# Performance work log

Measured on AMD Instinct MI355X. Metric: run time of the kernel, lower is better.

The kernel has to match this reference:

```python
import jax, jax.numpy as jnp
import numpy as np

N = 50000
E = 800000
NUM_GRAPHS = 64
D_IN = 261
D_SAGE = 64
D_LIN = 32
N_SAGE_REST = 6
N_LIN_REST = 3
EPS = 1e-5


def _layernorm(x, g, b):
    mu = jnp.mean(x, axis=-1, keepdims=True)
    var = jnp.mean((x - mu) ** 2, axis=-1, keepdims=True)
    return (x - mu) * jax.lax.rsqrt(var + EPS) * g + b


def _sage_block(x, Wl, bl, Wr, g, b, src, dst, inv_deg, residual):
    # mean aggregation of neighbor (source) features onto targets
    msum = jax.ops.segment_sum(x[src], dst, num_segments=N)  # [N, d]
    mean = msum * inv_deg  # [N, d]
    f = mean @ Wl + bl + x @ Wr  # lin_l(aggr) + lin_r(x); lin_r has no bias
    f = jax.nn.gelu(f, approximate=False)
    f = _layernorm(f, g, b)
    if residual:
        f = f + x
    return f


def _lin_block(x, W, b, g, beta, residual):
    f = jax.nn.gelu(x @ W + b, approximate=False)
    f = _layernorm(f, g, beta)
    if residual:
        f = f + x
    return f


def setup_inputs() -> dict:
    key = jax.random.key(0)
    ks = jax.random.split(key, 24)
    x = jax.random.normal(ks[0], (N, D_IN), dtype=jnp.float32)
    edge_index = jax.random.randint(ks[1], (2, E), 0, N, dtype=jnp.int64)
    batch = jnp.sort(jax.random.randint(ks[2], (N,), 0, NUM_GRAPHS, dtype=jnp.int64))

    def glorot(k, shape):
        fan_in = shape[0]
        return jax.random.normal(k, shape, dtype=jnp.float32) / np.sqrt(fan_in)

    inp = {
        "x": x, "edge_index": edge_index, "batch": batch,
        # first SAGE block (261 -> 64, no residual)
        "Wl0": glorot(ks[3], (D_IN, D_SAGE)), "bl0": jnp.zeros((D_SAGE,), jnp.float32),
        "Wr0": glorot(ks[4], (D_IN, D_SAGE)),
        "g0": jnp.ones((D_SAGE,), jnp.float32), "beta0": jnp.zeros((D_SAGE,), jnp.float32),
        # 6 residual SAGE blocks (64 -> 64), stacked
        "Wl": glorot(ks[5], (N_SAGE_REST, D_SAGE, D_SAGE)),
        "bl": jnp.zeros((N_SAGE_REST, D_SAGE), jnp.float32),
        "Wr": glorot(ks[6], (N_SAGE_REST, D_SAGE, D_SAGE)),
        "g": jnp.ones((N_SAGE_REST, D_SAGE), jnp.float32),
        "beta": jnp.zeros((N_SAGE_REST, D_SAGE), jnp.float32),
        # MLP: first LinearBlock 64 -> 32 (no residual)
        "M0": glorot(ks[7], (D_SAGE, D_LIN)), "mb0": jnp.zeros((D_LIN,), jnp.float32),
        "mg0": jnp.ones((D_LIN,), jnp.float32), "mbeta0": jnp.zeros((D_LIN,), jnp.float32),
        # 3 residual LinearBlocks 32 -> 32, stacked
        "M": glorot(ks[8], (N_LIN_REST, D_LIN, D_LIN)),
        "mb": jnp.zeros((N_LIN_REST, D_LIN), jnp.float32),
        "mg": jnp.ones((N_LIN_REST, D_LIN), jnp.float32),
        "mbeta": jnp.zeros((N_LIN_REST, D_LIN), jnp.float32),
        # final Linear 32 -> 1
        "Wf": glorot(ks[9], (D_LIN, 1)), "bf": jnp.zeros((1,), jnp.float32),
    }
    return inp


def reference(x, edge_index, batch, Wl0, bl0, Wr0, g0, beta0, Wl, bl, Wr, g, beta,
              M0, mb0, mg0, mbeta0, M, mb, mg, mbeta, Wf, bf):
    src, dst = edge_index[0], edge_index[1]
    deg = jax.ops.segment_sum(jnp.ones((E,), x.dtype), dst, num_segments=N)
    inv_deg = (1.0 / jnp.maximum(deg, 1.0))[:, None]  # [N,1]

    h = _sage_block(x, Wl0, bl0, Wr0, g0, beta0, src, dst, inv_deg, residual=False)
    for i in range(N_SAGE_REST):
        h = _sage_block(h, Wl[i], bl[i], Wr[i], g[i], beta[i], src, dst, inv_deg, residual=True)

    pooled = jax.ops.segment_sum(h, batch, num_segments=NUM_GRAPHS)  # [G, 64]

    m = _lin_block(pooled, M0, mb0, mg0, mbeta0, residual=False)
    for i in range(N_LIN_REST):
        m = _lin_block(m, M[i], mb[i], mg[i], mbeta[i], residual=True)
    return m @ Wf + bf  # [G, 1]
```

## Files before the change

### kernel.cpp

```cpp
#include <hip/hip_runtime.h>
#include <hip/hip_bf16.h>
#include <math.h>

#define N_NODES 50000
#define N_EDGES 800000
#define NUM_GRAPHS 64
#define NPAD 50048
#define KPAD0 288
#define PSPLIT 16
#define MAXDEG 64

#define G0_GRID    (NPAD / 32)
#define LAYER_GRID (NPAD / 32)
#define PREPW_TOT  (128 * KPAD0 + 6 * 128 * 64)
#define PREPW_GRID ((PREPW_TOT + 255) / 256)
#define CONV_GRID  (NPAD * (KPAD0 / 8) / 256)
#define PREP2_GRID (CONV_GRID + PREPW_GRID)

#define SLICES 8
#define NPS 6250
#define SCHUNK 2048
#define SCHUNKS ((N_EDGES + SCHUNK - 1) / SCHUNK)
#define SCAT_SPLIT 196

typedef __attribute__((ext_vector_type(8))) short short8;
typedef __attribute__((ext_vector_type(4))) float f32x4;

__device__ __forceinline__ float gelu_f(float v) {
    return 0.5f * v * (1.0f + erff(v * 0.70710678118654752440f));
}

__device__ __forceinline__ float half_sum32(float v) {
    v += __shfl_xor(v, 1); v += __shfl_xor(v, 2); v += __shfl_xor(v, 4);
    v += __shfl_xor(v, 8); v += __shfl_xor(v, 16);
    return v;
}

__device__ __forceinline__ float group_sum8(float v) {
    v += __shfl_xor(v, 1); v += __shfl_xor(v, 2); v += __shfl_xor(v, 4);
    return v;
}

__device__ __forceinline__ unsigned short f2bf(float f) {
    unsigned int u = __float_as_uint(f);
    unsigned int r = (u + 0x7fffu + ((u >> 16) & 1u)) >> 16;
    return (unsigned short)r;
}

__device__ __forceinline__ float bf_lo(unsigned int u) {
    return __uint_as_float(u << 16);
}
__device__ __forceinline__ float bf_hi(unsigned int u) {
    return __uint_as_float(u & 0xffff0000u);
}


__global__ __launch_bounds__(256) void k_prep2(
        const float* __restrict__ X, unsigned short* __restrict__ Xbf,
        const float* __restrict__ Wl0, const float* __restrict__ Wr0,
        const float* __restrict__ Wl, const float* __restrict__ Wr,
        unsigned short* __restrict__ Bt0, unsigned short* __restrict__ BtR) {
    const int blk = blockIdx.x;
    const int tid = threadIdx.x;
    if (blk < CONV_GRID) {
        int t = blk * 256 + tid;
        int node = t / (KPAD0 / 8);
        int k8 = (t - node * (KPAD0 / 8)) * 8;
        short8 v8;
        if (node < N_NODES) {
            #pragma unroll
            for (int j = 0; j < 8; ++j) {
                int k = k8 + j;
                float val = (k < 261) ? __builtin_nontemporal_load(&X[(size_t)node * 261 + k]) : 0.0f;
                v8[j] = (short)f2bf(val);
            }
        } else {
            #pragma unroll
            for (int j = 0; j < 8; ++j) v8[j] = 0;
        }
        *(short8*)&Xbf[(size_t)node * KPAD0 + k8] = v8;
        return;
    }
    int idx = (blk - CONV_GRID) * 256 + tid;
    const int n0 = 128 * KPAD0;
    if (idx < n0) {
        int j = idx / KPAD0, k = idx - j * KPAD0;
        float v = 0.0f;
        if (k < 261) v = (j < 64) ? Wl0[k * 64 + j] : Wr0[k * 64 + (j - 64)];
        Bt0[idx] = f2bf(v);
    } else if (idx < PREPW_TOT) {
        int r = idx - n0;
        int l = r >> 13;
        int rr = r & 8191;
        int j = rr >> 6, k = rr & 63;
        float v = (j < 64) ? Wl[l * 4096 + k * 64 + j] : Wr[l * 4096 + k * 64 + (j - 64)];
        BtR[r] = f2bf(v);
    }
}


__global__ __launch_bounds__(256) void k_scat(
        int cbase,
        const int* __restrict__ src, const int* __restrict__ dst,
        int* __restrict__ deg, unsigned short* __restrict__ col64) {
    const int sid = cbase * 8 + blockIdx.x;
    const int s = sid & (SLICES - 1);
    const int c = sid >> 3;
    const int base = c * SCHUNK;
    const int lim = min(base + SCHUNK, N_EDGES);
    for (int i = base + (int)threadIdx.x; i < lim; i += 256) {
        int d = __builtin_nontemporal_load(&dst[i]);
        if (d / NPS == s) {
            int sv = __builtin_nontemporal_load(&src[i]);
            int pos = atomicAdd(&deg[d], 1);
            if (pos < MAXDEG) col64[(d << 6) + pos] = (unsigned short)sv;
        }
    }
}


__global__ __launch_bounds__(256) void k_gemm0(
        const unsigned short* __restrict__ Xbf, const unsigned short* __restrict__ Bt0,
        unsigned short* __restrict__ U, float* __restrict__ V) {
    __shared__ __align__(16) unsigned short sB[64 * 296];
    const int tid = threadIdx.x;
    const int lane = tid & 63, wid = tid >> 6;
    const int l16 = lane & 15, quad = lane >> 4;
    const int ch = blockIdx.x & 1;
    const int m0 = (blockIdx.x >> 1) * 64;
    #pragma unroll
    for (int k = 0; k < 9; ++k) {
        int g = k * 256 + tid;
        int row = g / 36;
        int part = (g - row * 36) * 8;
        *(short8*)&sB[row * 296 + part] =
            *(const short8*)&Bt0[(size_t)(ch * 64 + row) * KPAD0 + part];
    }
    f32x4 acc[4];
    #pragma unroll
    for (int j = 0; j < 4; ++j) { acc[j][0] = 0.f; acc[j][1] = 0.f; acc[j][2] = 0.f; acc[j][3] = 0.f; }
    const unsigned short* xr = Xbf + (size_t)(m0 + wid * 16 + l16) * KPAD0 + quad * 8;
    __syncthreads();
    for (int kc = 0; kc < KPAD0; kc += 32) {
        short8 af = *(const short8*)(xr + kc);
        #pragma unroll
        for (int j = 0; j < 4; ++j) {
            short8 bfv = *(const short8*)&sB[(j * 16 + l16) * 296 + kc + quad * 8];
            acc[j] = __builtin_amdgcn_mfma_f32_16x16x32_bf16(af, bfv, acc[j], 0, 0, 0);
        }
    }
    const int rbase = m0 + wid * 16 + quad * 4;
    if (ch == 0) {
        #pragma unroll
        for (int j = 0; j < 4; ++j)
            #pragma unroll
            for (int r = 0; r < 4; ++r)
                U[(size_t)(rbase + r) * 64 + j * 16 + l16] = f2bf(acc[j][r]);
    } else {
        #pragma unroll
        for (int j = 0; j < 4; ++j)
            #pragma unroll
            for (int r = 0; r < 4; ++r)
                V[(size_t)(rbase + r) * 64 + j * 16 + l16] = acc[j][r];
    }
}


__global__ __launch_bounds__(256) void k_layer(
        const unsigned short* __restrict__ U_in, const float* __restrict__ V_in,
        unsigned short* __restrict__ h,
        const int* __restrict__ deg, const unsigned short* __restrict__ col64,
        const float* __restrict__ bias, const float* __restrict__ gam,
        const float* __restrict__ bet,
        const unsigned short* __restrict__ Bt_next,
        unsigned short* __restrict__ U_out, float* __restrict__ V_out,
        const int* __restrict__ batch, float* __restrict__ pool_part,
        int residual, int have_gemm) {
    __shared__ __align__(16) unsigned short sA[2 * 32 * 32];
    __shared__ __align__(16) unsigned short sB[128 * 72];
    const int tid = threadIdx.x;
    const int lane = tid & 63, wid = tid >> 6;
    const int sub = lane >> 3, hl = lane & 7;
    const int base = lane & 56;
    const int m0 = blockIdx.x * 32;
    const uint4* __restrict__ Up = (const uint4*)U_in;

    if (have_gemm) {
        #pragma unroll
        for (int k = 0; k < 4; ++k) {
            int g = k * 256 + tid;
            int row = g >> 3, part = (g & 7) * 8;
            *(short8*)&sB[row * 72 + part] = *(const short8*)&Bt_next[(size_t)row * 64 + part];
        }
    }

    const int nl = wid * 8 + sub;
    const int node = m0 + nl;
    const bool valid = (node < N_NODES);
    const int nd = valid ? node : 0;
    const int dg = valid ? deg[nd] : 0;
    const int cnt = min(dg, MAXDEG);
    uint4 cv = make_uint4(0u, 0u, 0u, 0u);
    if (valid) cv = *(const uint4*)&col64[((size_t)nd << 6) + hl * 8];

    float4 v0 = make_float4(0.f, 0.f, 0.f, 0.f), v1 = v0;
    if (valid) {
        v0 = *(const float4*)&V_in[(size_t)nd * 64 + 8 * hl];
        v1 = *(const float4*)&V_in[(size_t)nd * 64 + 8 * hl + 4];
    }
    uint4 hu = make_uint4(0u, 0u, 0u, 0u);
    if (residual && valid) hu = ((const uint4*)h)[(size_t)nd * 8 + hl];

    float s0 = 0.f, s1 = 0.f, s2 = 0.f, s3 = 0.f, s4 = 0.f, s5 = 0.f, s6 = 0.f, s7 = 0.f;
    for (int b = 0; b * 8 < cnt; b += 2) {
        #pragma unroll
        for (int hh = 0; hh < 2; ++hh) {
            const int sl = base + b + hh;
            unsigned int p0 = (unsigned int)__shfl((int)cv.x, sl);
            unsigned int p1 = (unsigned int)__shfl((int)cv.y, sl);
            unsigned int p2 = (unsigned int)__shfl((int)cv.z, sl);
            unsigned int p3 = (unsigned int)__shfl((int)cv.w, sl);
            const int eb = (b + hh) * 8;
            int c[8];
            c[0] = (int)(p0 & 0xffffu); c[1] = (int)(p0 >> 16);
            c[2] = (int)(p1 & 0xffffu); c[3] = (int)(p1 >> 16);
            c[4] = (int)(p2 & 0xffffu); c[5] = (int)(p2 >> 16);
            c[6] = (int)(p3 & 0xffffu); c[7] = (int)(p3 >> 16);
            #pragma unroll
            for (int i = 0; i < 8; ++i) {
                uint4 u = (eb + i < cnt) ? Up[(size_t)c[i] * 8 + hl] : make_uint4(0u, 0u, 0u, 0u);
                s0 += bf_lo(u.x); s1 += bf_hi(u.x);
                s2 += bf_lo(u.y); s3 += bf_hi(u.y);
                s4 += bf_lo(u.z); s5 += bf_hi(u.z);
                s6 += bf_lo(u.w); s7 += bf_hi(u.w);
            }
        }
    }
    const float id = 1.0f / fmaxf((float)dg, 1.0f);
    const float4 b0 = *(const float4*)&bias[8 * hl];
    const float4 b1 = *(const float4*)&bias[8 * hl + 4];
    float f0 = gelu_f(s0 * id + b0.x + v0.x);
    float f1 = gelu_f(s1 * id + b0.y + v0.y);
    float f2 = gelu_f(s2 * id + b0.z + v0.z);
    float f3 = gelu_f(s3 * id + b0.w + v0.w);
    float f4 = gelu_f(s4 * id + b1.x + v1.x);
    float f5 = gelu_f(s5 * id + b1.y + v1.y);
    float f6 = gelu_f(s6 * id + b1.z + v1.z);
    float f7 = gelu_f(s7 * id + b1.w + v1.w);
    float mu = group_sum8(((f0 + f1) + (f2 + f3)) + ((f4 + f5) + (f6 + f7))) * 0.015625f;
    float d0 = f0 - mu, d1 = f1 - mu, d2 = f2 - mu, d3 = f3 - mu;
    float d4 = f4 - mu, d5 = f5 - mu, d6 = f6 - mu, d7 = f7 - mu;
    float var = group_sum8(((d0 * d0 + d1 * d1) + (d2 * d2 + d3 * d3)) +
                           ((d4 * d4 + d5 * d5) + (d6 * d6 + d7 * d7))) * 0.015625f;
    float rs = rsqrtf(var + 1e-5f);
    const float4 g0v = *(const float4*)&gam[8 * hl];
    const float4 g1v = *(const float4*)&gam[8 * hl + 4];
    const float4 e0v = *(const float4*)&bet[8 * hl];
    const float4 e1v = *(const float4*)&bet[8 * hl + 4];
    f0 = d0 * rs * g0v.x + e0v.x;
    f1 = d1 * rs * g0v.y + e0v.y;
    f2 = d2 * rs * g0v.z + e0v.z;
    f3 = d3 * rs * g0v.w + e0v.w;
    f4 = d4 * rs * g1v.x + e1v.x;
    f5 = d5 * rs * g1v.y + e1v.y;
    f6 = d6 * rs * g1v.z + e1v.z;
    f7 = d7 * rs * g1v.w + e1v.w;
    if (residual && valid) {
        f0 += bf_lo(hu.x); f1 += bf_hi(hu.x);
        f2 += bf_lo(hu.y); f3 += bf_hi(hu.y);
        f4 += bf_lo(hu.z); f5 += bf_hi(hu.z);
        f6 += bf_lo(hu.w); f7 += bf_hi(hu.w);
    }

    if (pool_part) {
        const int myg = valid ? batch[nd] : -1;
        const int i_lo = (m0 < N_NODES) ? m0 : (N_NODES - 1);
        const int i_hi = (m0 + 31 < N_NODES) ? (m0 + 31) : (N_NODES - 1);
        const int g_lo = batch[i_lo];
        const int g_hi = batch[i_hi];
        const int split = blockIdx.x & (PSPLIT - 1);
        for (int g = g_lo; g <= g_hi; ++g) {
            const bool mine = (myg == g);
            float p0 = mine ? f0 : 0.f, p1 = mine ? f1 : 0.f;
            float p2 = mine ? f2 : 0.f, p3 = mine ? f3 : 0.f;
            float p4 = mine ? f4 : 0.f, p5 = mine ? f5 : 0.f;
            float p6 = mine ? f6 : 0.f, p7 = mine ? f7 : 0.f;
            p0 += __shfl_xor(p0, 8);  p1 += __shfl_xor(p1, 8);
            p2 += __shfl_xor(p2, 8);  p3 += __shfl_xor(p3, 8);
            p4 += __shfl_xor(p4, 8);  p5 += __shfl_xor(p5, 8);
            p6 += __shfl_xor(p6, 8);  p7 += __shfl_xor(p7, 8);
            p0 += __shfl_xor(p0, 16); p1 += __shfl_xor(p1, 16);
            p2 += __shfl_xor(p2, 16); p3 += __shfl_xor(p3, 16);
            p4 += __shfl_xor(p4, 16); p5 += __shfl_xor(p5, 16);
            p6 += __shfl_xor(p6, 16); p7 += __shfl_xor(p7, 16);
            p0 += __shfl_xor(p0, 32); p1 += __shfl_xor(p1, 32);
            p2 += __shfl_xor(p2, 32); p3 += __shfl_xor(p3, 32);
            p4 += __shfl_xor(p4, 32); p5 += __shfl_xor(p5, 32);
            p6 += __shfl_xor(p6, 32); p7 += __shfl_xor(p7, 32);
            if (sub == 0) {
                float* dp = &pool_part[((size_t)g * PSPLIT + split) * 64 + 8 * hl];
                atomicAdd(dp + 0, p0); atomicAdd(dp + 1, p1);
                atomicAdd(dp + 2, p2); atomicAdd(dp + 3, p3);
                atomicAdd(dp + 4, p4); atomicAdd(dp + 5, p5);
                atomicAdd(dp + 6, p6); atomicAdd(dp + 7, p7);
            }
        }
        return;
    }

    uint4 outw;
    outw.x = (unsigned int)f2bf(f0) | ((unsigned int)f2bf(f1) << 16);
    outw.y = (unsigned int)f2bf(f2) | ((unsigned int)f2bf(f3) << 16);
    outw.z = (unsigned int)f2bf(f4) | ((unsigned int)f2bf(f5) << 16);
    outw.w = (unsigned int)f2bf(f6) | ((unsigned int)f2bf(f7) << 16);
    if (valid) ((uint4*)h)[(size_t)nd * 8 + hl] = outw;
    *(uint4*)&sA[(((hl >> 2) * 32 + nl) << 5) + (hl & 3) * 8] = outw;

    if (!have_gemm) return;
    __syncthreads();

    const int l16 = lane & 15, quad = lane >> 4;
    const int wrow = wid & 1, colh = wid >> 1;
    f32x4 acc[4];
    #pragma unroll
    for (int j = 0; j < 4; ++j) { acc[j][0] = 0.f; acc[j][1] = 0.f; acc[j][2] = 0.f; acc[j][3] = 0.f; }
    #pragma unroll
    for (int kc = 0; kc < 64; kc += 32) {
        short8 af = *(const short8*)&sA[(((kc >> 5) * 32 + wrow * 16 + l16) << 5) + quad * 8];
        #pragma unroll
        for (int j = 0; j < 4; ++j) {
            short8 bfv = *(const short8*)&sB[(colh * 64 + j * 16 + l16) * 72 + kc + quad * 8];
            acc[j] = __builtin_amdgcn_mfma_f32_16x16x32_bf16(af, bfv, acc[j], 0, 0, 0);
        }
    }
    const int rbase = m0 + wrow * 16 + quad * 4;
    if (colh == 0) {
        #pragma unroll
        for (int j = 0; j < 4; ++j)
            #pragma unroll
            for (int r = 0; r < 4; ++r)
                U_out[(size_t)(rbase + r) * 64 + j * 16 + l16] = f2bf(acc[j][r]);
    } else {
        #pragma unroll
        for (int j = 0; j < 4; ++j)
            #pragma unroll
            for (int r = 0; r < 4; ++r)
                V_out[(size_t)(rbase + r) * 64 + j * 16 + l16] = acc[j][r];
    }
}


__global__ __launch_bounds__(1024) void k_head(const float* __restrict__ partial,
                                               const float* __restrict__ M0, const float* __restrict__ mb0,
                                               const float* __restrict__ mg0, const float* __restrict__ mbeta0,
                                               const float* __restrict__ M, const float* __restrict__ mb,
                                               const float* __restrict__ mg, const float* __restrict__ mbeta,
                                               const float* __restrict__ Wf, const float* __restrict__ bf,
                                               float* __restrict__ out) {
    __shared__ float sP[64 * 64];
    __shared__ float sA[64 * 33];
    __shared__ float sB[64 * 33];
    const int tx = threadIdx.x, ty = threadIdx.y;
    const int tid = ty * 32 + tx;
    for (int i = tid; i < 64 * 64; i += 1024) {
        int g = i >> 6, f = i & 63;
        float s = 0.0f;
        #pragma unroll
        for (int s2 = 0; s2 < PSPLIT; ++s2) s += partial[(size_t)(g * PSPLIT + s2) * 64 + f];
        sP[i] = s;
    }
    __syncthreads();
    #pragma unroll
    for (int rr = 0; rr < 2; ++rr) {
        int r = ty + rr * 32;
        float a = mb0[tx];
        for (int k = 0; k < 64; ++k) a += sP[r * 64 + k] * M0[k * 32 + tx];
        a = gelu_f(a);
        float mu = half_sum32(a) * (1.0f / 32.0f);
        float d = a - mu;
        float var = half_sum32(d * d) * (1.0f / 32.0f);
        a = d * rsqrtf(var + 1e-5f) * mg0[tx] + mbeta0[tx];
        sA[r * 33 + tx] = a;
    }
    __syncthreads();
    float* cur = sA;
    float* nxt = sB;
    for (int L = 0; L < 3; ++L) {
        const float* Mi = M + L * 32 * 32;
        const float* mbi = mb + L * 32;
        const float* mgi = mg + L * 32;
        const float* mbetai = mbeta + L * 32;
        #pragma unroll
        for (int rr = 0; rr < 2; ++rr) {
            int r = ty + rr * 32;
            float a = mbi[tx];
            for (int k = 0; k < 32; ++k) a += cur[r * 33 + k] * Mi[k * 32 + tx];
            a = gelu_f(a);
            float mu = half_sum32(a) * (1.0f / 32.0f);
            float d = a - mu;
            float var = half_sum32(d * d) * (1.0f / 32.0f);
            a = d * rsqrtf(var + 1e-5f) * mgi[tx] + mbetai[tx] + cur[r * 33 + tx];
            nxt[r * 33 + tx] = a;
        }
        __syncthreads();
        float* t = cur; cur = nxt; nxt = t;
    }
    #pragma unroll
    for (int rr = 0; rr < 2; ++rr) {
        int r = ty + rr * 32;
        float p = cur[r * 33 + tx] * Wf[tx];
        p = half_sum32(p);
        if (tx == 0) out[r] = p + bf[0];
    }
}


extern "C" void kernel_launch(void* const* d_in, const int* in_sizes, int n_in,
                              void* d_out, int out_size, void* d_ws, size_t ws_size,
                              hipStream_t stream) {
    const int N = N_NODES;
    const int E = N_EDGES;

    const float* x    = (const float*)d_in[0];
    const int* eidx   = (const int*)d_in[1];
    const int* batch  = (const int*)d_in[2];
    const float* Wl0  = (const float*)d_in[3];
    const float* bl0  = (const float*)d_in[4];
    const float* Wr0  = (const float*)d_in[5];
    const float* g0   = (const float*)d_in[6];
    const float* bet0 = (const float*)d_in[7];
    const float* Wl   = (const float*)d_in[8];
    const float* bl   = (const float*)d_in[9];
    const float* Wr   = (const float*)d_in[10];
    const float* gR   = (const float*)d_in[11];
    const float* betR = (const float*)d_in[12];
    const float* M0   = (const float*)d_in[13];
    const float* mb0  = (const float*)d_in[14];
    const float* mg0  = (const float*)d_in[15];
    const float* mbe0 = (const float*)d_in[16];
    const float* M    = (const float*)d_in[17];
    const float* mb   = (const float*)d_in[18];
    const float* mg   = (const float*)d_in[19];
    const float* mbe  = (const float*)d_in[20];
    const float* Wf   = (const float*)d_in[21];
    const float* bf   = (const float*)d_in[22];

    const int* src = eidx;
    const int* dst = eidx + E;

    char* p = (char*)d_ws;
    auto alloc = [&](size_t bytes) -> void* {
        void* q = (void*)p;
        p += (bytes + 255) & ~(size_t)255;
        return q;
    };
    int*   deg     = (int*)alloc((size_t)N * 4);
    float* partial = (float*)alloc((size_t)NUM_GRAPHS * PSPLIT * 64 * 4);
    unsigned short* col64 = (unsigned short*)alloc((size_t)N * MAXDEG * 2);
    unsigned short* Bt0 = (unsigned short*)alloc((size_t)128 * KPAD0 * 2);
    unsigned short* BtR = (unsigned short*)alloc((size_t)6 * 128 * 64 * 2);
    unsigned short* Xbf = (unsigned short*)alloc((size_t)NPAD * KPAD0 * 2);
    unsigned short* Ua  = (unsigned short*)alloc((size_t)NPAD * 64 * 2);
    unsigned short* Ub  = (unsigned short*)alloc((size_t)NPAD * 64 * 2);
    float* Va   = (float*)alloc((size_t)NPAD * 64 * 4);
    float* Vb   = (float*)alloc((size_t)NPAD * 64 * 4);
    unsigned short* hbuf = (unsigned short*)alloc((size_t)NPAD * 64 * 2);

    size_t zspan = (size_t)((char*)col64 - (char*)deg);
    hipMemsetAsync(deg, 0, zspan, stream);

    k_prep2<<<PREP2_GRID, 256, 0, stream>>>(x, Xbf, Wl0, Wr0, Wl, Wr, Bt0, BtR);

    k_scat<<<SCAT_SPLIT * 8, 256, 0, stream>>>(0, src, dst, deg, col64);
    k_scat<<<(SCHUNKS - SCAT_SPLIT) * 8, 256, 0, stream>>>(SCAT_SPLIT, src, dst, deg, col64);

    k_gemm0<<<G0_GRID, 256, 0, stream>>>(Xbf, Bt0, Ua, Va);

    unsigned short* Uin = Ua;  float* Vin = Va;
    unsigned short* Uout = Ub; float* Vout = Vb;
    for (int i = 0; i < 7; ++i) {
        const float* bias = (i == 0) ? bl0  : bl  + (size_t)(i - 1) * 64;
        const float* gam  = (i == 0) ? g0   : gR  + (size_t)(i - 1) * 64;
        const float* bet  = (i == 0) ? bet0 : betR + (size_t)(i - 1) * 64;
        const int have_gemm = (i < 6);
        float* pool_part = (i == 6) ? partial : nullptr;
        k_layer<<<LAYER_GRID, 256, 0, stream>>>(
            Uin, Vin, hbuf, deg, col64, bias, gam, bet,
            have_gemm ? (BtR + (size_t)i * 128 * 64) : BtR,
            Uout, Vout, batch, pool_part, (i > 0) ? 1 : 0, have_gemm);
        unsigned short* tu = Uin; Uin = Uout; Uout = tu;
        float* tv = Vin; Vin = Vout; Vout = tv;
    }

    k_head<<<1, dim3(32, 32), 0, stream>>>(partial, M0, mb0, mg0, mbe0, M, mb, mg, mbe, Wf, bf, (float*)d_out);
}
```

Measured before the change: 415.7 us.

## Fuse seven per-layer SAGE kernels into one persistent cooperative kernel with grid sync

Replaces the seven separate layer launches with one cooperative persistent kernel that loops over layers, processes node tiles in a grid-stride loop, and uses grid.sync between layers. It also merges the two scatter launches into one. The aim is to remove per-launch overhead and tail effects between layers. In exchange, the grid is capped by occupancy, tiles are processed serially per block, and a grid-wide barrier is added per layer.

```diff
diff --git a/kernel.cpp b/kernel.cpp
--- a/kernel.cpp
+++ b/kernel.cpp
@@ -1,4 +1,5 @@
 #include <hip/hip_runtime.h>
+#include <hip/hip_cooperative_groups.h>
 #include <hip/hip_bf16.h>
 #include <math.h>
 
@@ -11,7 +12,7 @@
 #define MAXDEG 64
 
 #define G0_GRID    (NPAD / 32)
-#define LAYER_GRID (NPAD / 32)
+#define LAYER_TILES (NPAD / 32)
 #define PREPW_TOT  (128 * KPAD0 + 6 * 128 * 64)
 #define PREPW_GRID ((PREPW_TOT + 255) / 256)
 #define CONV_GRID  (NPAD * (KPAD0 / 8) / 256)
@@ -21,7 +22,9 @@
 #define NPS 6250
 #define SCHUNK 2048
 #define SCHUNKS ((N_EDGES + SCHUNK - 1) / SCHUNK)
-#define SCAT_SPLIT 196
+#define SCAT_GRID (SCHUNKS * SLICES)
+
+namespace cg = cooperative_groups;
 
 typedef __attribute__((ext_vector_type(8))) short short8;
 typedef __attribute__((ext_vector_type(4))) float f32x4;
@@ -100,12 +103,10 @@
 
 
 __global__ __launch_bounds__(256) void k_scat(
-        int cbase,
         const int* __restrict__ src, const int* __restrict__ dst,
         int* __restrict__ deg, unsigned short* __restrict__ col64) {
-    const int sid = cbase * 8 + blockIdx.x;
-    const int s = sid & (SLICES - 1);
-    const int c = sid >> 3;
+    const int s = blockIdx.x & (SLICES - 1);
+    const int c = blockIdx.x >> 3;
     const int base = c * SCHUNK;
     const int lim = min(base + SCHUNK, N_EDGES);
     for (int i = base + (int)threadIdx.x; i < lim; i += 256) {
@@ -166,186 +167,202 @@
 }
 
 
-__global__ __launch_bounds__(256) void k_layer(
-        const unsigned short* __restrict__ U_in, const float* __restrict__ V_in,
+__global__ __launch_bounds__(256) void k_net(
+        unsigned short* __restrict__ Ua, float* __restrict__ Va,
+        unsigned short* __restrict__ Ub, float* __restrict__ Vb,
         unsigned short* __restrict__ h,
         const int* __restrict__ deg, const unsigned short* __restrict__ col64,
-        const float* __restrict__ bias, const float* __restrict__ gam,
-        const float* __restrict__ bet,
-        const unsigned short* __restrict__ Bt_next,
-        unsigned short* __restrict__ U_out, float* __restrict__ V_out,
-        const int* __restrict__ batch, float* __restrict__ pool_part,
-        int residual, int have_gemm) {
+        const float* __restrict__ bl0, const float* __restrict__ g0,
+        const float* __restrict__ bet0,
+        const float* __restrict__ blR, const float* __restrict__ gR,
+        const float* __restrict__ betR,
+        const unsigned short* __restrict__ BtR,
+        const int* __restrict__ batch, float* __restrict__ partial) {
     __shared__ __align__(16) unsigned short sA[2 * 32 * 32];
     __shared__ __align__(16) unsigned short sB[128 * 72];
+    cg::grid_group grid = cg::this_grid();
     const int tid = threadIdx.x;
     const int lane = tid & 63, wid = tid >> 6;
     const int sub = lane >> 3, hl = lane & 7;
     const int base = lane & 56;
-    const int m0 = blockIdx.x * 32;
-    const uint4* __restrict__ Up = (const uint4*)U_in;
-
-    if (have_gemm) {
-        #pragma unroll
-        for (int k = 0; k < 4; ++k) {
-            int g = k * 256 + tid;
-            int row = g >> 3, part = (g & 7) * 8;
-            *(short8*)&sB[row * 72 + part] = *(const short8*)&Bt_next[(size_t)row * 64 + part];
-        }
-    }
-
-    const int nl = wid * 8 + sub;
-    const int node = m0 + nl;
-    const bool valid = (node < N_NODES);
-    const int nd = valid ? node : 0;
-    const int dg = valid ? deg[nd] : 0;
-    const int cnt = min(dg, MAXDEG);
-    uint4 cv = make_uint4(0u, 0u, 0u, 0u);
-    if (valid) cv = *(const uint4*)&col64[((size_t)nd << 6) + hl * 8];
-
-    float4 v0 = make_float4(0.f, 0.f, 0.f, 0.f), v1 = v0;
-    if (valid) {
-        v0 = *(const float4*)&V_in[(size_t)nd * 64 + 8 * hl];
-        v1 = *(const float4*)&V_in[(size_t)nd * 64 + 8 * hl + 4];
-    }
-    uint4 hu = make_uint4(0u, 0u, 0u, 0u);
-    if (residual && valid) hu = ((const uint4*)h)[(size_t)nd * 8 + hl];
-
-    float s0 = 0.f, s1 = 0.f, s2 = 0.f, s3 = 0.f, s4 = 0.f, s5 = 0.f, s6 = 0.f, s7 = 0.f;
-    for (int b = 0; b * 8 < cnt; b += 2) {
-        #pragma unroll
-        for (int hh = 0; hh < 2; ++hh) {
-            const int sl = base + b + hh;
-            unsigned int p0 = (unsigned int)__shfl((int)cv.x, sl);
-            unsigned int p1 = (unsigned int)__shfl((int)cv.y, sl);
-            unsigned int p2 = (unsigned int)__shfl((int)cv.z, sl);
-            unsigned int p3 = (unsigned int)__shfl((int)cv.w, sl);
-            const int eb = (b + hh) * 8;
-            int c[8];
-            c[0] = (int)(p0 & 0xffffu); c[1] = (int)(p0 >> 16);
-            c[2] = (int)(p1 & 0xffffu); c[3] = (int)(p1 >> 16);
-            c[4] = (int)(p2 & 0xffffu); c[5] = (int)(p2 >> 16);
-            c[6] = (int)(p3 & 0xffffu); c[7] = (int)(p3 >> 16);
+
+    for (int L = 0; L < 7; ++L) {
+        const int have_gemm = (L < 6);
+        const int residual = (L > 0);
+        const unsigned short* U_in = (L & 1) ? Ub : Ua;
+        const float* V_in = (L & 1) ? Vb : Va;
+        unsigned short* U_out = (L & 1) ? Ua : Ub;
+        float* V_out = (L & 1) ? Va : Vb;
+        const float* bias = L ? (blR + (size_t)(L - 1) * 64) : bl0;
+        const float* gam  = L ? (gR  + (size_t)(L - 1) * 64) : g0;
+        const float* bet  = L ? (betR + (size_t)(L - 1) * 64) : bet0;
+        const uint4* __restrict__ Up = (const uint4*)U_in;
+
+        if (have_gemm) {
+            const unsigned short* Bt = BtR + (size_t)L * 128 * 64;
             #pragma unroll
-            for (int i = 0; i < 8; ++i) {
-                uint4 u = (eb + i < cnt) ? Up[(size_t)c[i] * 8 + hl] : make_uint4(0u, 0u, 0u, 0u);
-                s0 += bf_lo(u.x); s1 += bf_hi(u.x);
-                s2 += bf_lo(u.y); s3 += bf_hi(u.y);
-                s4 += bf_lo(u.z); s5 += bf_hi(u.z);
-                s6 += bf_lo(u.w); s7 += bf_hi(u.w);
+            for (int k = 0; k < 4; ++k) {
+                int g = k * 256 + tid;
+                int row = g >> 3, part = (g & 7) * 8;
+                *(short8*)&sB[row * 72 + part] = *(const short8*)&Bt[(size_t)row * 64 + part];
             }
         }
-    }
-    const float id = 1.0f / fmaxf((float)dg, 1.0f);
-    const float4 b0 = *(const float4*)&bias[8 * hl];
-    const float4 b1 = *(const float4*)&bias[8 * hl + 4];
-    float f0 = gelu_f(s0 * id + b0.x + v0.x);
-    float f1 = gelu_f(s1 * id + b0.y + v0.y);
-    float f2 = gelu_f(s2 * id + b0.z + v0.z);
-    float f3 = gelu_f(s3 * id + b0.w + v0.w);
-    float f4 = gelu_f(s4 * id + b1.x + v1.x);
-    float f5 = gelu_f(s5 * id + b1.y + v1.y);
-    float f6 = gelu_f(s6 * id + b1.z + v1.z);
-    float f7 = gelu_f(s7 * id + b1.w + v1.w);
-    float mu = group_sum8(((f0 + f1) + (f2 + f3)) + ((f4 + f5) + (f6 + f7))) * 0.015625f;
-    float d0 = f0 - mu, d1 = f1 - mu, d2 = f2 - mu, d3 = f3 - mu;
-    float d4 = f4 - mu, d5 = f5 - mu, d6 = f6 - mu, d7 = f7 - mu;
-    float var = group_sum8(((d0 * d0 + d1 * d1) + (d2 * d2 + d3 * d3)) +
-                           ((d4 * d4 + d5 * d5) + (d6 * d6 + d7 * d7))) * 0.015625f;
-    float rs = rsqrtf(var + 1e-5f);
-    const float4 g0v = *(const float4*)&gam[8 * hl];
-    const float4 g1v = *(const float4*)&gam[8 * hl + 4];
-    const float4 e0v = *(const float4*)&bet[8 * hl];
-    const float4 e1v = *(const float4*)&bet[8 * hl + 4];
-    f0 = d0 * rs * g0v.x + e0v.x;
-    f1 = d1 * rs * g0v.y + e0v.y;
-    f2 = d2 * rs * g0v.z + e0v.z;
-    f3 = d3 * rs * g0v.w + e0v.w;
-    f4 = d4 * rs * g1v.x + e1v.x;
-    f5 = d5 * rs * g1v.y + e1v.y;
-    f6 = d6 * rs * g1v.z + e1v.z;
-    f7 = d7 * rs * g1v.w + e1v.w;
-    if (residual && valid) {
-        f0 += bf_lo(hu.x); f1 += bf_hi(hu.x);
-        f2 += bf_lo(hu.y); f3 += bf_hi(hu.y);
-        f4 += bf_lo(hu.z); f5 += bf_hi(hu.z);
-        f6 += bf_lo(hu.w); f7 += bf_hi(hu.w);
-    }
-
-    if (pool_part) {
-        const int myg = valid ? batch[nd] : -1;
-        const int i_lo = (m0 < N_NODES) ? m0 : (N_NODES - 1);
-        const int i_hi = (m0 + 31 < N_NODES) ? (m0 + 31) : (N_NODES - 1);
-        const int g_lo = batch[i_lo];
-        const int g_hi = batch[i_hi];
-        const int split = blockIdx.x & (PSPLIT - 1);
-        for (int g = g_lo; g <= g_hi; ++g) {
-            const bool mine = (myg == g);
-            float p0 = mine ? f0 : 0.f, p1 = mine ? f1 : 0.f;
-            float p2 = mine ? f2 : 0.f, p3 = mine ? f3 : 0.f;
-            float p4 = mine ? f4 : 0.f, p5 = mine ? f5 : 0.f;
-            float p6 = mine ? f6 : 0.f, p7 = mine ? f7 : 0.f;
-            p0 += __shfl_xor(p0, 8);  p1 += __shfl_xor(p1, 8);
-            p2 += __shfl_xor(p2, 8);  p3 += __shfl_xor(p3, 8);
-            p4 += __shfl_xor(p4, 8);  p5 += __shfl_xor(p5, 8);
-            p6 += __shfl_xor(p6, 8);  p7 += __shfl_xor(p7, 8);
-            p0 += __shfl_xor(p0, 16); p1 += __shfl_xor(p1, 16);
-            p2 += __shfl_xor(p2, 16); p3 += __shfl_xor(p3, 16);
-            p4 += __shfl_xor(p4, 16); p5 += __shfl_xor(p5, 16);
-            p6 += __shfl_xor(p6, 16); p7 += __shfl_xor(p7, 16);
-            p0 += __shfl_xor(p0, 32); p1 += __shfl_xor(p1, 32);
-            p2 += __shfl_xor(p2, 32); p3 += __shfl_xor(p3, 32);
-            p4 += __shfl_xor(p4, 32); p5 += __shfl_xor(p5, 32);
-            p6 += __shfl_xor(p6, 32); p7 += __shfl_xor(p7, 32);
-            if (sub == 0) {
-                float* dp = &pool_part[((size_t)g * PSPLIT + split) * 64 + 8 * hl];
-                atomicAdd(dp + 0, p0); atomicAdd(dp + 1, p1);
-                atomicAdd(dp + 2, p2); atomicAdd(dp + 3, p3);
-                atomicAdd(dp + 4, p4); atomicAdd(dp + 5, p5);
-                atomicAdd(dp + 6, p6); atomicAdd(dp + 7, p7);
+
+        for (int tile = blockIdx.x; tile < LAYER_TILES; tile += gridDim.x) {
+            const int m0 = tile * 32;
+            const int nl = wid * 8 + sub;
+            const int node = m0 + nl;
+            const bool valid = (node < N_NODES);
+            const int nd = valid ? node : 0;
+            const int dg = valid ? deg[nd] : 0;
+            const int cnt = min(dg, MAXDEG);
+            uint4 cv = make_uint4(0u, 0u, 0u, 0u);
+            if (valid) cv = *(const uint4*)&col64[((size_t)nd << 6) + hl * 8];
+
+            float4 v0 = make_float4(0.f, 0.f, 0.f, 0.f), v1 = v0;
+            if (valid) {
+                v0 = *(const float4*)&V_in[(size_t)nd * 64 + 8 * hl];
+                v1 = *(const float4*)&V_in[(size_t)nd * 64 + 8 * hl + 4];
+            }
+            uint4 hu = make_uint4(0u, 0u, 0u, 0u);
+            if (residual && valid) hu = ((const uint4*)h)[(size_t)nd * 8 + hl];
+
+            float s0 = 0.f, s1 = 0.f, s2 = 0.f, s3 = 0.f, s4 = 0.f, s5 = 0.f, s6 = 0.f, s7 = 0.f;
+            for (int b = 0; b * 8 < cnt; b += 2) {
+                #pragma unroll
+                for (int hh = 0; hh < 2; ++hh) {
+                    const int sl = base + b + hh;
+                    unsigned int p0 = (unsigned int)__shfl((int)cv.x, sl);
+                    unsigned int p1 = (unsigned int)__shfl((int)cv.y, sl);
+                    unsigned int p2 = (unsigned int)__shfl((int)cv.z, sl);
+                    unsigned int p3 = (unsigned int)__shfl((int)cv.w, sl);
+                    const int eb = (b + hh) * 8;
+                    int c[8];
+                    c[0] = (int)(p0 & 0xffffu); c[1] = (int)(p0 >> 16);
+                    c[2] = (int)(p1 & 0xffffu); c[3] = (int)(p1 >> 16);
+                    c[4] = (int)(p2 & 0xffffu); c[5] = (int)(p2 >> 16);
+                    c[6] = (int)(p3 & 0xffffu); c[7] = (int)(p3 >> 16);
+                    #pragma unroll
+                    for (int i = 0; i < 8; ++i) {
+                        uint4 u = (eb + i < cnt) ? Up[(size_t)c[i] * 8 + hl] : make_uint4(0u, 0u, 0u, 0u);
+                        s0 += bf_lo(u.x); s1 += bf_hi(u.x);
+                        s2 += bf_lo(u.y); s3 += bf_hi(u.y);
+                        s4 += bf_lo(u.z); s5 += bf_hi(u.z);
+                        s6 += bf_lo(u.w); s7 += bf_hi(u.w);
+                    }
+                }
+            }
+            const float id = 1.0f / fmaxf((float)dg, 1.0f);
+            const float4 b0 = *(const float4*)&bias[8 * hl];
+            const float4 b1 = *(const float4*)&bias[8 * hl + 4];
+            float f0 = gelu_f(s0 * id + b0.x + v0.x);
+            float f1 = gelu_f(s1 * id + b0.y + v0.y);
+            float f2 = gelu_f(s2 * id + b0.z + v0.z);
+            float f3 = gelu_f(s3 * id + b0.w + v0.w);
+            float f4 = gelu_f(s4 * id + b1.x + v1.x);
+            float f5 = gelu_f(s5 * id + b1.y + v1.y);
+            float f6 = gelu_f(s6 * id + b1.z + v1.z);
+            float f7 = gelu_f(s7 * id + b1.w + v1.w);
+            float mu = group_sum8(((f0 + f1) + (f2 + f3)) + ((f4 + f5) + (f6 + f7))) * 0.015625f;
+            float d0 = f0 - mu, d1 = f1 - mu, d2 = f2 - mu, d3 = f3 - mu;
+            float d4 = f4 - mu, d5 = f5 - mu, d6 = f6 - mu, d7 = f7 - mu;
+            float var = group_sum8(((d0 * d0 + d1 * d1) + (d2 * d2 + d3 * d3)) +
+                                   ((d4 * d4 + d5 * d5) + (d6 * d6 + d7 * d7))) * 0.015625f;
+            float rs = rsqrtf(var + 1e-5f);
+            const float4 g0v = *(const float4*)&gam[8 * hl];
+            const float4 g1v = *(const float4*)&gam[8 * hl + 4];
+            const float4 e0v = *(const float4*)&bet[8 * hl];
+            const float4 e1v = *(const float4*)&bet[8 * hl + 4];
+            f0 = d0 * rs * g0v.x + e0v.x;
+            f1 = d1 * rs * g0v.y + e0v.y;
+            f2 = d2 * rs * g0v.z + e0v.z;
+            f3 = d3 * rs * g0v.w + e0v.w;
+            f4 = d4 * rs * g1v.x + e1v.x;
+            f5 = d5 * rs * g1v.y + e1v.y;
+            f6 = d6 * rs * g1v.z + e1v.z;
+            f7 = d7 * rs * g1v.w + e1v.w;
+            if (residual && valid) {
+                f0 += bf_lo(hu.x); f1 += bf_hi(hu.x);
+                f2 += bf_lo(hu.y); f3 += bf_hi(hu.y);
+                f4 += bf_lo(hu.z); f5 += bf_hi(hu.z);
+                f6 += bf_lo(hu.w); f7 += bf_hi(hu.w);
+            }
+
+            if (L == 6) {
+                const int myg = valid ? batch[nd] : -1;
+                const int i_lo = (m0 < N_NODES) ? m0 : (N_NODES - 1);
+                const int i_hi = (m0 + 31 < N_NODES) ? (m0 + 31) : (N_NODES - 1);
+                const int g_lo = batch[i_lo];
+                const int g_hi = batch[i_hi];
+                const int split = tile & (PSPLIT - 1);
+                for (int g = g_lo; g <= g_hi; ++g) {
+                    const bool mine = (myg == g);
+                    float p0 = mine ? f0 : 0.f, p1 = mine ? f1 : 0.f;
+                    float p2 = mine ? f2 : 0.f, p3 = mine ? f3 : 0.f;
+                    float p4 = mine ? f4 : 0.f, p5 = mine ? f5 : 0.f;
+                    float p6 = mine ? f6 : 0.f, p7 = mine ? f7 : 0.f;
+                    p0 += __shfl_xor(p0, 8);  p1 += __shfl_xor(p1, 8);
+                    p2 += __shfl_xor(p2, 8);  p3 += __shfl_xor(p3, 8);
+                    p4 += __shfl_xor(p4, 8);  p5 += __shfl_xor(p5, 8);
+                    p6 += __shfl_xor(p6, 8);  p7 += __shfl_xor(p7, 8);
+                    p0 += __shfl_xor(p0, 16); p1 += __shfl_xor(p1, 16);
+                    p2 += __shfl_xor(p2, 16); p3 += __shfl_xor(p3, 16);
+                    p4 += __shfl_xor(p4, 16); p5 += __shfl_xor(p5, 16);
+                    p6 += __shfl_xor(p6, 16); p7 += __shfl_xor(p7, 16);
+                    p0 += __shfl_xor(p0, 32); p1 += __shfl_xor(p1, 32);
+                    p2 += __shfl_xor(p2, 32); p3 += __shfl_xor(p3, 32);
+                    p4 += __shfl_xor(p4, 32); p5 += __shfl_xor(p5, 32);
+                    p6 += __shfl_xor(p6, 32); p7 += __shfl_xor(p7, 32);
+                    if (sub == 0) {
+                        float* dp = &partial[((size_t)g * PSPLIT + split) * 64 + 8 * hl];
+                        atomicAdd(dp + 0, p0); atomicAdd(dp + 1, p1);
+                        atomicAdd(dp + 2, p2); atomicAdd(dp + 3, p3);
+                        atomicAdd(dp + 4, p4); atomicAdd(dp + 5, p5);
+                        atomicAdd(dp + 6, p6); atomicAdd(dp + 7, p7);
+                    }
+                }
+            } else {
+                uint4 outw;
+                outw.x = (unsigned int)f2bf(f0) | ((unsigned int)f2bf(f1) << 16);
+                outw.y = (unsigned int)f2bf(f2) | ((unsigned int)f2bf(f3) << 16);
+                outw.z = (unsigned int)f2bf(f4) | ((unsigned int)f2bf(f5) << 16);
+                outw.w = (unsigned int)f2bf(f6) | ((unsigned int)f2bf(f7) << 16);
+                if (valid) ((uint4*)h)[(size_t)nd * 8 + hl] = outw;
+                *(uint4*)&sA[(((hl >> 2) * 32 + nl) << 5) + (hl & 3) * 8] = outw;
+                __syncthreads();
+
+                const int l16 = lane & 15, quad = lane >> 4;
+                const int wrow = wid & 1, colh = wid >> 1;
+                f32x4 acc[4];
+                #pragma unroll
+                for (int j = 0; j < 4; ++j) { acc[j][0] = 0.f; acc[j][1] = 0.f; acc[j][2] = 0.f; acc[j][3] = 0.f; }
+                #pragma unroll
+                for (int kc = 0; kc < 64; kc += 32) {
+                    short8 af = *(const short8*)&sA[(((kc >> 5) * 32 + wrow * 16 + l16) << 5) + quad * 8];
+                    #pragma unroll
+                    for (int j = 0; j < 4; ++j) {
+                        short8 bfv = *(const short8*)&sB[(colh * 64 + j * 16 + l16) * 72 + kc + quad * 8];
+                        acc[j] = __builtin_amdgcn_mfma_f32_16x16x32_bf16(af, bfv, acc[j], 0, 0, 0);
+                    }
+                }
+                const int rbase = m0 + wrow * 16 + quad * 4;
+                if (colh == 0) {
+                    #pragma unroll
+                    for (int j = 0; j < 4; ++j)
+                        #pragma unroll
+                        for (int r = 0; r < 4; ++r)
+                            U_out[(size_t)(rbase + r) * 64 + j * 16 + l16] = f2bf(acc[j][r]);
+                } else {
+                    #pragma unroll
+                    for (int j = 0; j < 4; ++j)
+                        #pragma unroll
+                        for (int r = 0; r < 4; ++r)
+                            V_out[(size_t)(rbase + r) * 64 + j * 16 + l16] = acc[j][r];
+                }
+                __syncthreads();
             }
         }
-        return;
-    }
-
-    uint4 outw;
-    outw.x = (unsigned int)f2bf(f0) | ((unsigned int)f2bf(f1) << 16);
-    outw.y = (unsigned int)f2bf(f2) | ((unsigned int)f2bf(f3) << 16);
-    outw.z = (unsigned int)f2bf(f4) | ((unsigned int)f2bf(f5) << 16);
-    outw.w = (unsigned int)f2bf(f6) | ((unsigned int)f2bf(f7) << 16);
-    if (valid) ((uint4*)h)[(size_t)nd * 8 + hl] = outw;
-    *(uint4*)&sA[(((hl >> 2) * 32 + nl) << 5) + (hl & 3) * 8] = outw;
-
-    if (!have_gemm) return;
-    __syncthreads();
-
-    const int l16 = lane & 15, quad = lane >> 4;
-    const int wrow = wid & 1, colh = wid >> 1;
-    f32x4 acc[4];
-    #pragma unroll
-    for (int j = 0; j < 4; ++j) { acc[j][0] = 0.f; acc[j][1] = 0.f; acc[j][2] = 0.f; acc[j][3] = 0.f; }
-    #pragma unroll
-    for (int kc = 0; kc < 64; kc += 32) {
-        short8 af = *(const short8*)&sA[(((kc >> 5) * 32 + wrow * 16 + l16) << 5) + quad * 8];
-        #pragma unroll
-        for (int j = 0; j < 4; ++j) {
-            short8 bfv = *(const short8*)&sB[(colh * 64 + j * 16 + l16) * 72 + kc + quad * 8];
-            acc[j] = __builtin_amdgcn_mfma_f32_16x16x32_bf16(af, bfv, acc[j], 0, 0, 0);
-        }
-    }
-    const int rbase = m0 + wrow * 16 + quad * 4;
-    if (colh == 0) {
-        #pragma unroll
-        for (int j = 0; j < 4; ++j)
-            #pragma unroll
-            for (int r = 0; r < 4; ++r)
-                U_out[(size_t)(rbase + r) * 64 + j * 16 + l16] = f2bf(acc[j][r]);
-    } else {
-        #pragma unroll
-        for (int j = 0; j < 4; ++j)
-            #pragma unroll
-            for (int r = 0; r < 4; ++r)
-                V_out[(size_t)(rbase + r) * 64 + j * 16 + l16] = acc[j][r];
+        grid.sync();
     }
 }
 
@@ -471,26 +488,20 @@
 
     k_prep2<<<PREP2_GRID, 256, 0, stream>>>(x, Xbf, Wl0, Wr0, Wl, Wr, Bt0, BtR);
 
-    k_scat<<<SCAT_SPLIT * 8, 256, 0, stream>>>(0, src, dst, deg, col64);
-    k_scat<<<(SCHUNKS - SCAT_SPLIT) * 8, 256, 0, stream>>>(SCAT_SPLIT, src, dst, deg, col64);
+    k_scat<<<SCAT_GRID, 256, 0, stream>>>(src, dst, deg, col64);
 
     k_gemm0<<<G0_GRID, 256, 0, stream>>>(Xbf, Bt0, Ua, Va);
 
-    unsigned short* Uin = Ua;  float* Vin = Va;
-    unsigned short* Uout = Ub; float* Vout = Vb;
-    for (int i = 0; i < 7; ++i) {
-        const float* bias = (i == 0) ? bl0  : bl  + (size_t)(i - 1) * 64;
-        const float* gam  = (i == 0) ? g0   : gR  + (size_t)(i - 1) * 64;
-        const float* bet  = (i == 0) ? bet0 : betR + (size_t)(i - 1) * 64;
-        const int have_gemm = (i < 6);
-        float* pool_part = (i == 6) ? partial : nullptr;
-        k_layer<<<LAYER_GRID, 256, 0, stream>>>(
-            Uin, Vin, hbuf, deg, col64, bias, gam, bet,
-            have_gemm ? (BtR + (size_t)i * 128 * 64) : BtR,
-            Uout, Vout, batch, pool_part, (i > 0) ? 1 : 0, have_gemm);
-        unsigned short* tu = Uin; Uin = Uout; Uout = tu;
-        float* tv = Vin; Vin = Vout; Vout = tv;
-    }
+    int occ = 0;
+    if (hipOccupancyMaxActiveBlocksPerMultiprocessor(&occ, (const void*)k_net, 256, 0) != hipSuccess || occ <= 0)
+        occ = 4;
+    int grid = occ * 256;
+    if (grid > LAYER_TILES) grid = LAYER_TILES;
+    void* args[] = { (void*)&Ua, (void*)&Va, (void*)&Ub, (void*)&Vb, (void*)&hbuf,
+                     (void*)&deg, (void*)&col64, (void*)&bl0, (void*)&g0, (void*)&bet0,
+                     (void*)&bl, (void*)&gR, (void*)&betR, (void*)&BtR,
+                     (void*)&batch, (void*)&partial };
+    hipLaunchCooperativeKernel((void*)k_net, dim3(grid), dim3(256), args, 0, stream);
 
     k_head<<<1, dim3(32, 32), 0, stream>>>(partial, M0, mb0, mg0, mbe0, M, mb, mg, mbe, Wf, bf, (float*)d_out);
 }
```

Result: slower. 768.6 us (+84.9%).
